# Optimization experiments

Hardware: AMD Instinct MI355X
Metric: run time of the kernel (lower is better)

The kernel has to match this reference:

```python
import jax, jax.numpy as jnp
import numpy as np

B, C, H, W = 16, 256, 64, 64
OUT_C = 3
N_TOKENS = 512
N_RES = 3
RED = 4
CB = C // RED  # bottleneck channels in ResChain
DN = ('NCHW', 'OIHW', 'NCHW')


def _conv(x, w, pad):
    return jax.lax.conv_general_dilated(x, w, (1, 1), pad, dimension_numbers=DN)


def setup_inputs() -> dict:
    key = jax.random.key(0)
    ks = jax.random.split(key, 8)
    return {
        'input': jax.random.normal(ks[0], (B, C, H, W), jnp.float32),
        'embed': jax.random.normal(ks[1], (C, N_TOKENS), jnp.float32),  # Quantize codebook [dim, n_embed]
        'res_w1': jax.random.normal(ks[2], (N_RES, CB, C, 3, 3), jnp.float32) * 0.02,
        'res_b1': jnp.zeros((N_RES, CB), jnp.float32),
        'res_w2': jax.random.normal(ks[3], (N_RES, C, CB, 1, 1), jnp.float32) * 0.02,
        'res_b2': jnp.zeros((N_RES, C), jnp.float32),
        'out_w': jax.random.normal(ks[4], (OUT_C, C, 1, 1), jnp.float32) * 0.02,
        'out_b': jnp.zeros((OUT_C,), jnp.float32),
    }


def reference(input, embed, res_w1, res_b1, res_w2, res_b2, out_w, out_b):
    sg = jax.lax.stop_gradient
    # --- Quantize (VQ-VAE codebook lookup, straight-through) ---
    x = jnp.transpose(input, (0, 2, 3, 1))  # [B,H,W,C]
    flat = x.reshape(-1, C)                  # [N, C]
    # squared L2 distance to each code: ||f||^2 - 2 f.e + ||e||^2
    dist = (flat * flat).sum(-1, keepdims=True) - 2.0 * (flat @ embed) + (embed * embed).sum(0)
    idx = jnp.argmin(dist, axis=-1).reshape(B, H, W)        # [B,H,W] int
    quantize = jnp.take(embed.T, idx, axis=0)               # embed_code: [B,H,W,C]
    diff = jnp.mean((sg(quantize) - x) ** 2)
    quantize = x + sg(quantize - x)                         # straight-through
    q = jnp.transpose(quantize, (0, 3, 1, 2))               # [B,C,H,W]
    # --- dec: ResChain(n_res_block) + 1x1 conv ---
    for i in range(N_RES):
        h = jax.nn.relu(q)
        h = _conv(h, res_w1[i], 'SAME') + res_b1[i][None, :, None, None]
        h = jax.nn.relu(h)
        h = _conv(h, res_w2[i], 'VALID') + res_b2[i][None, :, None, None]
        q = q + h
    quant = _conv(q, out_w, 'VALID') + out_b[None, :, None, None]  # [B,OUT_C,H,W]
    # --- wordfreq: per-batch bincount over idx (no grad) ---
    flat_idx = idx.reshape(B, -1)
    seg = (flat_idx + jnp.arange(B, dtype=flat_idx.dtype)[:, None] * N_TOKENS).reshape(-1)
    counts = jax.ops.segment_sum(jnp.ones_like(seg, jnp.float32), seg, num_segments=B * N_TOKENS)
    wordfreq = counts.reshape(B, N_TOKENS) / float(H * W)
    return quant, diff.reshape(1), wordfreq
```

## Files before the change

### kernel.cpp

```cpp
#include <hip/hip_runtime.h>


typedef __attribute__((ext_vector_type(8))) short short8;
typedef __attribute__((ext_vector_type(16))) float f32x16;
typedef __attribute__((ext_vector_type(8))) _Float16 half8;
typedef __attribute__((ext_vector_type(2))) _Float16 half2_t;
typedef unsigned short ushort_t;
typedef unsigned long long u64;

#define WS_QA    0
#define WS_QB    8388608
#define WS_ET    16777216
#define WS_EN    16842752
#define WS_EPK   16843264
#define WS_W1PK  16908800
#define WS_W2PK  17129984
#define WS_DIFF  17154560
#define WS_TOK   17154568
#define WS_DST   17220104
#define WS_FN    17285640
#define WS_WL    17351176

#define MARGIN 0.12f

__device__ inline ushort_t f2bf(float f) {
  unsigned u = __float_as_uint(f);
  return (ushort_t)((u + 0x7fffu + ((u >> 16) & 1u)) >> 16);
}
__device__ inline float bf2f(ushort_t h) { return __uint_as_float(((unsigned)h) << 16); }
union HU { _Float16 h; ushort_t u; };
union S8H { short8 s; half8 h; half2_t h2[4]; };

__global__ __launch_bounds__(256) void prep_kernel(
    const float* __restrict__ embed, const float* __restrict__ w1,
    const float* __restrict__ w2, float* __restrict__ ws, float* __restrict__ wf) {
  int i = blockIdx.x * 256 + threadIdx.x;
  if (i < 131072) {
    int t = i >> 8, c = i & 255;
    ((ushort_t*)(ws + WS_ET))[i] = f2bf(embed[c * 512 + t]);
  }
  if (i < 512) {
    float s = 0.f;
    for (int c = 0; c < 256; ++c) { float v = embed[c * 512 + i]; s += v * v; }
    ws[WS_EN + i] = s;
  }
  if (i < 131072) {
    int j = i & 7, lane = (i >> 3) & 63, at = (i >> 9) & 15, ks = i >> 13;
    int code = at * 32 + (lane & 31);
    int c = ks * 16 + (lane >> 5) * 8 + j;
    HU cv; cv.h = (_Float16)embed[c * 512 + code];
    ((ushort_t*)(ws + WS_EPK))[i] = cv.u;
  }
  if (i < 442368) {
    int j = i & 7; int lane = (i >> 3) & 63; int of = (i >> 9) & 1;
    int k16 = (i >> 10) & 15; int rest = i >> 14;
    int tap = rest % 9; int layer = rest / 9;
    int oc = of * 32 + (lane & 31);
    int c = k16 * 16 + (lane >> 5) * 8 + j;
    ((ushort_t*)(ws + WS_W1PK))[i] = f2bf(w1[((layer * 64 + oc) * 256 + c) * 9 + tap]);
  }
  if (i < 49152) {
    int j = i & 7, lane = (i >> 3) & 63, at = (i >> 9) & 7, ks = (i >> 12) & 3, l = i >> 14;
    int co = at * 32 + (lane & 31), cb = ks * 16 + (lane >> 5) * 8 + j;
    ((ushort_t*)(ws + WS_W2PK))[i] = f2bf(w2[(l * 256 + co) * 64 + cb]);
  }
  if (i < 8192) wf[i] = 0.f;
  if (i == 0) { ws[WS_DIFF] = 0.f; ((int*)(ws + WS_WL))[0] = 0; }
}

__global__ __launch_bounds__(512, 4) void dist_kernel(
    const float* __restrict__ input, const half8* __restrict__ epk,
    const float* __restrict__ enorm, int* __restrict__ tok,
    float* __restrict__ dst, float* __restrict__ fnv, int* __restrict__ wl) {
  __shared__ __align__(16) ushort_t sfp[2048 * 8];
  __shared__ float senorm[512];
  __shared__ float trim1[512], trim2[512];
  __shared__ int   trii[512];

  int blk = blockIdx.x, b = blk >> 6, hw0 = (blk & 63) << 6;
  int tid = threadIdx.x, lane = tid & 63, wave = tid >> 6;
  senorm[tid] = enorm[tid];

  {
    int cg = tid >> 3, sub = tid & 7;
    int ks_s = cg >> 2, hi_s = (cg >> 1) & 1, jq = cg & 1;
    const float* src0 = input + ((size_t)(b * 256 + cg * 4)) * 4096 + hw0 + sub * 8;
    float vv[4][8];
#pragma unroll
    for (int m = 0; m < 4; ++m) {
      const float4* s4 = (const float4*)(src0 + (size_t)m * 4096);
      float4 aa = s4[0], bb = s4[1];
      vv[m][0] = aa.x; vv[m][1] = aa.y; vv[m][2] = aa.z; vv[m][3] = aa.w;
      vv[m][4] = bb.x; vv[m][5] = bb.y; vv[m][6] = bb.z; vv[m][7] = bb.w;
    }
    u64* sfp64 = (u64*)sfp;
#pragma unroll
    for (int i = 0; i < 8; ++i) {
      int pl = sub * 8 + i;
      int bt = pl >> 5, lw = (pl & 31) + 32 * hi_s;
      u64 pk = 0;
#pragma unroll
      for (int m = 0; m < 4; ++m) {
        HU cv; cv.h = (_Float16)vv[m][i];
        pk |= ((u64)cv.u) << (16 * m);
      }
      sfp64[((bt * 16 + ks_s) * 64 + lw) * 2 + jq] = pk;
    }
  }
  __syncthreads();

  f32x16 acc[2][2];
#pragma unroll
  for (int bt = 0; bt < 2; ++bt)
#pragma unroll
    for (int a = 0; a < 2; ++a)
#pragma unroll
      for (int r = 0; r < 16; ++r) acc[bt][a][r] = 0.f;

  const short8* sfp8 = (const short8*)sfp;
  float fnp0 = 0.f, fnp1 = 0.f;
#pragma unroll 2
  for (int ks = 0; ks < 16; ++ks) {
    S8H u0, u1;
    u0.s = sfp8[ks * 64 + lane];
    u1.s = sfp8[(16 + ks) * 64 + lane];
#if __has_builtin(__builtin_amdgcn_fdot2)
#pragma unroll
    for (int k = 0; k < 4; ++k) {
      fnp0 = __builtin_amdgcn_fdot2(u0.h2[k], u0.h2[k], fnp0, false);
      fnp1 = __builtin_amdgcn_fdot2(u1.h2[k], u1.h2[k], fnp1, false);
    }
#else
#pragma unroll
    for (int k = 0; k < 8; ++k) {
      float v0 = (float)u0.h[k], v1 = (float)u1.h[k];
      fnp0 += v0 * v0; fnp1 += v1 * v1;
    }
#endif
#pragma unroll
    for (int a = 0; a < 2; ++a) {
      half8 ah = epk[(ks * 16 + wave * 2 + a) * 64 + lane];
      acc[0][a] = __builtin_amdgcn_mfma_f32_32x32x16_f16(ah, u0.h, acc[0][a], 0, 0, 0);
      acc[1][a] = __builtin_amdgcn_mfma_f32_32x32x16_f16(ah, u1.h, acc[1][a], 0, 0, 0);
    }
  }
  fnp0 += __shfl_xor(fnp0, 32, 64);
  fnp1 += __shfl_xor(fnp1, 32, 64);

  int hi5 = lane >> 5;
#pragma unroll
  for (int bt = 0; bt < 2; ++bt) {
    float m1 = 3.4e38f, m2 = 3.4e38f; int i1 = 0;
#pragma unroll
    for (int a = 0; a < 2; ++a)
#pragma unroll
      for (int r = 0; r < 16; ++r) {
        int code = (wave * 2 + a) * 32 + (r & 3) + 8 * (r >> 2) + 4 * hi5;
        float v = senorm[code] - 2.0f * acc[bt][a][r];
        if (v < m1) { m2 = m1; m1 = v; i1 = code; }
        else if (v < m2) m2 = v;
      }
    float o1 = __shfl_xor(m1, 32, 64);
    float o2 = __shfl_xor(m2, 32, 64);
    int   oi = __shfl_xor(i1, 32, 64);
    float n2 = fminf(fmaxf(m1, o1), fminf(m2, o2));
    float n1 = fminf(m1, o1);
    int   ni = (o1 < m1) ? oi : i1;
    if (lane < 32) {
      int p = bt * 32 + lane;
      trim1[p * 8 + wave] = n1; trim2[p * 8 + wave] = n2; trii[p * 8 + wave] = ni;
    }
  }
  __syncthreads();

  if (wave == 0) {
    int p = lane;
    float m1 = trim1[p * 8], m2 = trim2[p * 8]; int i1 = trii[p * 8];
#pragma unroll
    for (int w = 1; w < 8; ++w) {
      float a1 = trim1[p * 8 + w], a2 = trim2[p * 8 + w]; int ai = trii[p * 8 + w];
      float n2 = fminf(fmaxf(m1, a1), fminf(m2, a2));
      if (a1 < m1) { m1 = a1; i1 = ai; }
      m2 = n2;
    }
    float myfn = (lane < 32) ? fnp0 : fnp1;
    int gpos = blk * 64 + p;
    tok[gpos] = i1;
    dst[gpos] = myfn + m1;
    fnv[gpos] = myfn;
    bool flag = (m2 - m1 < MARGIN);
    u64 mk = __ballot(flag);
    int base = 0;
    if (lane == 0 && mk) base = atomicAdd(wl, (int)__popcll(mk));
    base = __shfl(base, 0, 64);
    if (flag) {
      int off = (int)__popcll(mk & ((1ull << lane) - 1ull));
      wl[1 + base + off] = gpos;
    }
  }
}

__global__ __launch_bounds__(256) void redo_kernel(
    const float* __restrict__ input, const float* __restrict__ embed,
    const float* __restrict__ enorm, const int* __restrict__ wl,
    int* __restrict__ tok, float* __restrict__ dst, const float* __restrict__ fnv) {
  __shared__ float sf[256], rv[256];
  __shared__ int   ri[256];
  int n = wl[0];
  int tid = threadIdx.x;
  for (int e = blockIdx.x; e < n; e += gridDim.x) {
    int gpos = wl[1 + e];
    int b = gpos >> 12, hw = gpos & 4095;
    sf[tid] = input[((size_t)(b * 256 + tid)) * 4096 + hw];
    __syncthreads();
    float d0 = 0.f, d1 = 0.f;
#pragma unroll 4
    for (int c = 0; c < 256; ++c) {
      float fv = sf[c];
      d0 += fv * embed[c * 512 + tid];
      d1 += fv * embed[c * 512 + 256 + tid];
    }
    float v0 = enorm[tid] - 2.f * d0;
    float v1 = enorm[256 + tid] - 2.f * d1;
    float bv; int bi;
    if (v1 < v0) { bv = v1; bi = 256 + tid; } else { bv = v0; bi = tid; }
    rv[tid] = bv; ri[tid] = bi;
    __syncthreads();
    for (int s = 128; s > 0; s >>= 1) {
      if (tid < s) {
        float ov = rv[tid + s]; int oi2 = ri[tid + s];
        if (ov < rv[tid] || (ov == rv[tid] && oi2 < ri[tid])) { rv[tid] = ov; ri[tid] = oi2; }
      }
      __syncthreads();
    }
    if (tid == 0) { tok[gpos] = ri[0]; dst[gpos] = fnv[gpos] + rv[0]; }
    __syncthreads();
  }
}

__global__ __launch_bounds__(256) void finalize_kernel(
    const int* __restrict__ tok, const float* __restrict__ dst,
    const ushort_t* __restrict__ embedT, float* __restrict__ wf,
    float* __restrict__ diffp, ushort_t* __restrict__ qout) {
  int blk = blockIdx.x;
  int tid = threadIdx.x, lane = tid & 63, wave = tid >> 6;
  int gbase = blk * 64;
  int b = gbase >> 12;
  if (wave == 0) {
    int t = tok[gbase + lane];
    atomicAdd(&wf[b * 512 + t], 1.0f / 4096.0f);
    float d = dst[gbase + lane];
#pragma unroll
    for (int off = 32; off >= 1; off >>= 1) d += __shfl_down(d, off, 64);
    if (lane == 0) atomicAdd(diffp, d);
  }
#pragma unroll 1
  for (int j = 0; j < 16; ++j) {
    int p = wave * 16 + j;
    int t = __builtin_amdgcn_readfirstlane(tok[gbase + p]);
    const u64* src = (const u64*)(embedT + (size_t)t * 256);
    u64* dstp = (u64*)(qout + ((size_t)(gbase + p)) * 256);
    dstp[lane] = src[lane];
  }
}

__global__ __launch_bounds__(512, 4) void fused_layer(
    const ushort_t* __restrict__ qin, ushort_t* __restrict__ qout,
    const ushort_t* __restrict__ w1pk, const float* __restrict__ b1,
    const ushort_t* __restrict__ w2pk, const float* __restrict__ b2, int l) {
  __shared__ __align__(16) char arena[38912];
  ushort_t* hbuf   = (ushort_t*)arena;
  float*    sb2    = (float*)(arena + 9728);
  short8*   stg    = (short8*)(arena + 10752);
  float*    red    = (float*)(arena + 10752);
  ushort_t* qstage = (ushort_t*)(arena + 10752);

  int blk = blockIdx.x;
  int b = blk >> 6; int t = blk & 63;
  int ty0 = (t >> 3) << 3;
  int tx0 = (t & 7) << 3;
  int tid = threadIdx.x, lane = tid & 63, w = tid >> 6;
  int pt = w & 1, ot = (w >> 1) & 1, kh = w >> 2;
  int l31 = lane & 31, kb5 = lane >> 5;

  if (tid < 256) sb2[tid] = b2[l * 256 + tid];

  const short8* wp  = (const short8*)w1pk + (size_t)l * 18432;
  const short8* w2p = (const short8*)w2pk;

  short8 sreg[2];
  auto loadch = [&](int cs) {
#pragma unroll
    for (int s = 0; s < 2; ++s) {
      int u = s * 512 + tid;
      if (u < 800) {
        int cg = u & 7; int pix = u >> 3; int y = pix / 10; int x = pix - y * 10;
        int sy = ty0 + y - 1, sx = tx0 + x - 1;
        if (sy >= 0 && sy < 64 && sx >= 0 && sx < 64) {
          sreg[s] = *(const short8*)(qin + ((size_t)(b * 4096 + sy * 64 + sx)) * 256 + cs * 64 + cg * 8);
        } else {
          short8 z;
#pragma unroll
          for (int k2 = 0; k2 < 8; ++k2) z[k2] = 0;
          sreg[s] = z;
        }
      }
    }
  };
  auto writech = [&](int buf) {
#pragma unroll
    for (int s = 0; s < 2; ++s) {
      int u = s * 512 + tid;
      if (u < 800) {
        int cg = u & 7; int pix = u >> 3; int y = pix / 10; int x = pix - y * 10;
        short8 sv = sreg[s];
#pragma unroll
        for (int k2 = 0; k2 < 8; ++k2) if (sv[k2] < 0) sv[k2] = 0;
        stg[buf * 880 + (y * 8 + cg) * 11 + x] = sv;
      }
    }
  };

  f32x16 acc;
#pragma unroll
  for (int r = 0; r < 16; ++r) acc[r] = 0.f;

  int py0 = pt * 4 + (l31 >> 3);
  int px0 = lane & 7;

  loadch(0);
  writech(0);
#pragma unroll 1
  for (int cs = 0; cs < 4; ++cs) {
    __syncthreads();
    if (cs < 3) loadch(cs + 1);
    int buf = cs & 1;
#pragma unroll 1
    for (int dy = 0; dy < 3; ++dy) {
#pragma unroll 1
      for (int dx = 0; dx < 3; ++dx) {
        int tap = dy * 3 + dx;
#pragma unroll
        for (int ks2 = 0; ks2 < 2; ++ks2) {
          int kk = kh * 2 + ks2;
          short8 A = stg[buf * 880 + ((py0 + dy) * 8 + kk * 2 + kb5) * 11 + px0 + dx];
          short8 B = wp[(tap * 16 + cs * 4 + kk) * 128 + ot * 64 + lane];
          acc = __builtin_amdgcn_mfma_f32_32x32x16_bf16(A, B, acc, 0, 0, 0);
        }
      }
    }
    if (cs < 3) writech((cs + 1) & 1);
  }
  __syncthreads();

  if (kh == 1) {
    float4* d = (float4*)(red + (w & 3) * 1024 + lane * 16);
#pragma unroll
    for (int r4 = 0; r4 < 4; ++r4) {
      float4 v; v.x = acc[r4 * 4]; v.y = acc[r4 * 4 + 1];
      v.z = acc[r4 * 4 + 2]; v.w = acc[r4 * 4 + 3];
      d[r4] = v;
    }
  }
  __syncthreads();
  if (kh == 0) {
    const float* s = red + (w & 3) * 1024 + lane * 16;
    int oc = ot * 32 + l31;
    float bb = b1[l * 64 + oc];
#pragma unroll
    for (int r = 0; r < 16; ++r) {
      int row = (r & 3) + 8 * (r >> 2) + 4 * kb5;
      hbuf[(pt * 32 + row) * 76 + oc] = f2bf(fmaxf(acc[r] + s[r] + bb, 0.f));
    }
  }
  __syncthreads();

  int pt2 = w & 1, coq = w >> 1;
#pragma unroll 1
  for (int ch = 0; ch < 2; ++ch) {
    short8 qv[2];
#pragma unroll
    for (int it = 0; it < 2; ++it) {
      int u = it * 512 + tid;
      int p = u >> 4, c8 = u & 15;
      int gy = ty0 + (p >> 3), gx = tx0 + (p & 7);
      qv[it] = *(const short8*)(qin + ((size_t)(b * 4096 + gy * 64 + gx)) * 256 + ch * 128 + c8 * 8);
    }

    f32x16 acc2;
#pragma unroll
    for (int r = 0; r < 16; ++r) acc2[r] = 0.f;
#pragma unroll
    for (int ks = 0; ks < 4; ++ks) {
      short8 A = *(const short8*)(hbuf + (pt2 * 32 + l31) * 76 + ks * 16 + kb5 * 8);
      short8 B = w2p[((l * 4 + ks) * 8 + ch * 4 + coq) * 64 + lane];
      acc2 = __builtin_amdgcn_mfma_f32_32x32x16_bf16(A, B, acc2, 0, 0, 0);
    }
    {
      int cc = coq * 32 + l31;
      float bb2 = sb2[ch * 128 + cc];
#pragma unroll
      for (int r = 0; r < 16; ++r) {
        int row = (r & 3) + 8 * (r >> 2) + 4 * kb5;
        qstage[(pt2 * 32 + row) * 136 + cc] = f2bf(acc2[r] + bb2);
      }
    }
    __syncthreads();
#pragma unroll
    for (int it = 0; it < 2; ++it) {
      int u = it * 512 + tid;
      int p = u >> 4, c8 = u & 15;
      short8 hv = *(const short8*)(qstage + p * 136 + c8 * 8);
      int gy = ty0 + (p >> 3), gx = tx0 + (p & 7);
      size_t gidx = ((size_t)(b * 4096 + gy * 64 + gx)) * 256 + ch * 128 + c8 * 8;
      short8 ov;
#pragma unroll
      for (int k2 = 0; k2 < 8; ++k2)
        ov[k2] = (short)f2bf(bf2f((ushort_t)qv[it][k2]) + bf2f((ushort_t)hv[k2]));
      *(short8*)(qout + gidx) = ov;
    }
    __syncthreads();
  }
}

__global__ __launch_bounds__(256) void final_kernel(
    const ushort_t* __restrict__ qbuf, const float* __restrict__ ow,
    const float* __restrict__ ob, float* __restrict__ out,
    const float* __restrict__ ws) {
  int t = blockIdx.x * 256 + threadIdx.x;
  int pos = t >> 4, c16 = t & 15;
  const ushort_t* qp = qbuf + (size_t)pos * 256 + c16 * 16;
  short8 v0 = *(const short8*)qp;
  short8 v1 = *(const short8*)(qp + 8);
  float a0 = 0.f, a1 = 0.f, a2 = 0.f;
#pragma unroll
  for (int k = 0; k < 16; ++k) {
    float f = bf2f((ushort_t)(k < 8 ? v0[k] : v1[k - 8]));
    int c = c16 * 16 + k;
    a0 += f * ow[c];
    a1 += f * ow[256 + c];
    a2 += f * ow[512 + c];
  }
#pragma unroll
  for (int off = 1; off < 16; off <<= 1) {
    a0 += __shfl_xor(a0, off, 64);
    a1 += __shfl_xor(a1, off, 64);
    a2 += __shfl_xor(a2, off, 64);
  }
  if (c16 == 0) {
    int b = pos >> 12, hw = pos & 4095;
    out[(b * 3 + 0) * 4096 + hw] = a0 + ob[0];
    out[(b * 3 + 1) * 4096 + hw] = a1 + ob[1];
    out[(b * 3 + 2) * 4096 + hw] = a2 + ob[2];
  }
  if (t == 0) out[196608] = ws[WS_DIFF] * (1.0f / 16777216.0f);
}

extern "C" void kernel_launch(void* const* d_in, const int* in_sizes, int n_in,
                              void* d_out, int out_size, void* d_ws, size_t ws_size,
                              hipStream_t stream) {
  (void)in_sizes; (void)n_in; (void)out_size; (void)ws_size;
  const float* input = (const float*)d_in[0];
  const float* embed = (const float*)d_in[1];
  const float* b1 = (const float*)d_in[3];
  const float* b2 = (const float*)d_in[5];
  const float* ow = (const float*)d_in[6];
  const float* ob = (const float*)d_in[7];
  float* ws = (float*)d_ws;
  float* out = (float*)d_out;
  float* wf = out + 196609;

  ushort_t* qA = (ushort_t*)(ws + WS_QA);
  ushort_t* qB = (ushort_t*)(ws + WS_QB);
  const ushort_t* et = (const ushort_t*)(ws + WS_ET);
  const half8* epk = (const half8*)(ws + WS_EPK);
  const ushort_t* w1pk = (const ushort_t*)(ws + WS_W1PK);
  const ushort_t* w2pk = (const ushort_t*)(ws + WS_W2PK);
  int*   tok = (int*)(ws + WS_TOK);
  float* dst = ws + WS_DST;
  float* fnv = ws + WS_FN;
  int*   wl  = (int*)(ws + WS_WL);

  hipLaunchKernelGGL(prep_kernel, dim3(1728), dim3(256), 0, stream,
                     embed, (const float*)d_in[2], (const float*)d_in[4], ws, wf);
  hipLaunchKernelGGL(dist_kernel, dim3(1024), dim3(512), 0, stream,
                     input, epk, ws + WS_EN, tok, dst, fnv, wl);
  hipLaunchKernelGGL(redo_kernel, dim3(1024), dim3(256), 0, stream,
                     input, embed, ws + WS_EN, wl, tok, dst, fnv);
  hipLaunchKernelGGL(finalize_kernel, dim3(1024), dim3(256), 0, stream,
                     tok, dst, et, wf, ws + WS_DIFF, qA);
  hipLaunchKernelGGL(fused_layer, dim3(1024), dim3(512), 0, stream,
                     qA, qB, w1pk, b1, w2pk, b2, 0);
  hipLaunchKernelGGL(fused_layer, dim3(1024), dim3(512), 0, stream,
                     qB, qA, w1pk, b1, w2pk, b2, 1);
  hipLaunchKernelGGL(fused_layer, dim3(1024), dim3(512), 0, stream,
                     qA, qB, w1pk, b1, w2pk, b2, 2);
  hipLaunchKernelGGL(final_kernel, dim3(4096), dim3(256), 0, stream,
                     qB, ow, ob, out, ws);
}
```

Before: 229.8 us.

## Replace first residual 3x3 conv with per-token lookup table of conv contributions

Since the first layer's input is a quantized codebook vector per pixel, the 3x3 conv of relu(q) is precomputed as a LUT [token][tap][oc] by a new small kernel, and layer 0 sums nine LUT rows per pixel instead of running the MFMA conv. This removes the bulk of layer-0 conv FLOPs in exchange for a serial LUT build (128 blocks over 256 channels) and gather-style LUT reads. Zero padding is handled by skipping out-of-bounds taps. fp32 accumulation of bf16-rounded embed values changes rounding slightly compared with the bf16 MFMA path.

```diff
diff --git a/kernel.cpp b/kernel.cpp
--- a/kernel.cpp
+++ b/kernel.cpp
@@ -20,6 +20,7 @@
 #define WS_DST   17220104
 #define WS_FN    17285640
 #define WS_WL    17351176
+#define WS_LUT   17416720
 
 #define MARGIN 0.12f
 
@@ -66,6 +67,26 @@
   }
   if (i < 8192) wf[i] = 0.f;
   if (i == 0) { ws[WS_DIFF] = 0.f; ((int*)(ws + WS_WL))[0] = 0; }
+}
+
+__global__ __launch_bounds__(256) void lut_kernel(
+    const float* __restrict__ embed, const float* __restrict__ w1,
+    float* __restrict__ lut) {
+  int g = blockIdx.x * 256 + threadIdx.x;
+  int t = g & 511, oc = g >> 9;
+  float acc[9];
+#pragma unroll
+  for (int tap = 0; tap < 9; ++tap) acc[tap] = 0.f;
+#pragma unroll 4
+  for (int c = 0; c < 256; ++c) {
+    float v = fmaxf(bf2f(f2bf(embed[c * 512 + t])), 0.f);
+    const float* wr = w1 + (size_t)(oc * 256 + c) * 9;
+#pragma unroll
+    for (int tap = 0; tap < 9; ++tap) acc[tap] += v * wr[tap];
+  }
+#pragma unroll
+  for (int tap = 0; tap < 9; ++tap)
+    lut[((size_t)t * 9 + tap) * 64 + oc] = acc[tap];
 }
 
 __global__ __launch_bounds__(512, 4) void dist_kernel(
@@ -264,6 +285,111 @@
   }
 }
 
+__global__ __launch_bounds__(512, 4) void layer0_kernel(
+    const ushort_t* __restrict__ qin, ushort_t* __restrict__ qout,
+    const int* __restrict__ tok, const float* __restrict__ lut,
+    const float* __restrict__ b1, const ushort_t* __restrict__ w2pk,
+    const float* __restrict__ b2) {
+  __shared__ __align__(16) char arena[28672];
+  ushort_t* hbuf   = (ushort_t*)arena;
+  float*    sb2    = (float*)(arena + 9728);
+  int*      stok   = (int*)(arena + 10752);
+  ushort_t* qstage = (ushort_t*)(arena + 11264);
+
+  int blk = blockIdx.x;
+  int b = blk >> 6; int t = blk & 63;
+  int ty0 = (t >> 3) << 3;
+  int tx0 = (t & 7) << 3;
+  int tid = threadIdx.x, lane = tid & 63, w = tid >> 6;
+  int l31 = lane & 31, kb5 = lane >> 5;
+
+  if (tid < 256) sb2[tid] = b2[tid];
+  if (tid < 100) {
+    int yy = tid / 10, xx = tid - yy * 10;
+    int sy = ty0 + yy - 1, sx = tx0 + xx - 1;
+    stok[tid] = (sy >= 0 && sy < 64 && sx >= 0 && sx < 64)
+              ? tok[b * 4096 + sy * 64 + sx] : -1;
+  }
+  __syncthreads();
+
+  {
+    int px = tid >> 3, oc8 = tid & 7;
+    int y = px >> 3, x = px & 7;
+    float a[8];
+    const float* bp = b1 + oc8 * 8;
+#pragma unroll
+    for (int j = 0; j < 8; ++j) a[j] = bp[j];
+#pragma unroll
+    for (int dy = 0; dy < 3; ++dy)
+#pragma unroll
+      for (int dx = 0; dx < 3; ++dx) {
+        int tt = stok[(y + dy) * 10 + (x + dx)];
+        if (tt >= 0) {
+          const float4* r = (const float4*)(lut + ((size_t)tt * 9 + dy * 3 + dx) * 64 + oc8 * 8);
+          float4 v0 = r[0], v1 = r[1];
+          a[0] += v0.x; a[1] += v0.y; a[2] += v0.z; a[3] += v0.w;
+          a[4] += v1.x; a[5] += v1.y; a[6] += v1.z; a[7] += v1.w;
+        }
+      }
+    u64 p0 = 0, p1 = 0;
+#pragma unroll
+    for (int j = 0; j < 4; ++j) p0 |= ((u64)f2bf(fmaxf(a[j], 0.f))) << (16 * j);
+#pragma unroll
+    for (int j = 0; j < 4; ++j) p1 |= ((u64)f2bf(fmaxf(a[4 + j], 0.f))) << (16 * j);
+    *(u64*)(hbuf + px * 76 + oc8 * 8) = p0;
+    *(u64*)(hbuf + px * 76 + oc8 * 8 + 4) = p1;
+  }
+  __syncthreads();
+
+  const short8* w2p = (const short8*)w2pk;
+  int pt2 = w & 1, coq = w >> 1;
+#pragma unroll 1
+  for (int ch = 0; ch < 2; ++ch) {
+    short8 qv[2];
+#pragma unroll
+    for (int it = 0; it < 2; ++it) {
+      int u = it * 512 + tid;
+      int p = u >> 4, c8 = u & 15;
+      int gy = ty0 + (p >> 3), gx = tx0 + (p & 7);
+      qv[it] = *(const short8*)(qin + ((size_t)(b * 4096 + gy * 64 + gx)) * 256 + ch * 128 + c8 * 8);
+    }
+
+    f32x16 acc2;
+#pragma unroll
+    for (int r = 0; r < 16; ++r) acc2[r] = 0.f;
+#pragma unroll
+    for (int ks = 0; ks < 4; ++ks) {
+      short8 A = *(const short8*)(hbuf + (pt2 * 32 + l31) * 76 + ks * 16 + kb5 * 8);
+      short8 B = w2p[(ks * 8 + ch * 4 + coq) * 64 + lane];
+      acc2 = __builtin_amdgcn_mfma_f32_32x32x16_bf16(A, B, acc2, 0, 0, 0);
+    }
+    {
+      int cc = coq * 32 + l31;
+      float bb2 = sb2[ch * 128 + cc];
+#pragma unroll
+      for (int r = 0; r < 16; ++r) {
+        int row = (r & 3) + 8 * (r >> 2) + 4 * kb5;
+        qstage[(pt2 * 32 + row) * 136 + cc] = f2bf(acc2[r] + bb2);
+      }
+    }
+    __syncthreads();
+#pragma unroll
+    for (int it = 0; it < 2; ++it) {
+      int u = it * 512 + tid;
+      int p = u >> 4, c8 = u & 15;
+      short8 hv = *(const short8*)(qstage + p * 136 + c8 * 8);
+      int gy = ty0 + (p >> 3), gx = tx0 + (p & 7);
+      size_t gidx = ((size_t)(b * 4096 + gy * 64 + gx)) * 256 + ch * 128 + c8 * 8;
+      short8 ov;
+#pragma unroll
+      for (int k2 = 0; k2 < 8; ++k2)
+        ov[k2] = (short)f2bf(bf2f((ushort_t)qv[it][k2]) + bf2f((ushort_t)hv[k2]));
+      *(short8*)(qout + gidx) = ov;
+    }
+    __syncthreads();
+  }
+}
+
 __global__ __launch_bounds__(512, 4) void fused_layer(
     const ushort_t* __restrict__ qin, ushort_t* __restrict__ qout,
     const ushort_t* __restrict__ w1pk, const float* __restrict__ b1,
@@ -462,6 +588,7 @@
   (void)in_sizes; (void)n_in; (void)out_size; (void)ws_size;
   const float* input = (const float*)d_in[0];
   const float* embed = (const float*)d_in[1];
+  const float* w1 = (const float*)d_in[2];
   const float* b1 = (const float*)d_in[3];
   const float* b2 = (const float*)d_in[5];
   const float* ow = (const float*)d_in[6];
@@ -480,17 +607,20 @@
   float* dst = ws + WS_DST;
   float* fnv = ws + WS_FN;
   int*   wl  = (int*)(ws + WS_WL);
+  float* lut = ws + WS_LUT;
 
   hipLaunchKernelGGL(prep_kernel, dim3(1728), dim3(256), 0, stream,
-                     embed, (const float*)d_in[2], (const float*)d_in[4], ws, wf);
+                     embed, w1, (const float*)d_in[4], ws, wf);
+  hipLaunchKernelGGL(lut_kernel, dim3(128), dim3(256), 0, stream,
+                     embed, w1, lut);
   hipLaunchKernelGGL(dist_kernel, dim3(1024), dim3(512), 0, stream,
                      input, epk, ws + WS_EN, tok, dst, fnv, wl);
   hipLaunchKernelGGL(redo_kernel, dim3(1024), dim3(256), 0, stream,
                      input, embed, ws + WS_EN, wl, tok, dst, fnv);
   hipLaunchKernelGGL(finalize_kernel, dim3(1024), dim3(256), 0, stream,
                      tok, dst, et, wf, ws + WS_DIFF, qA);
-  hipLaunchKernelGGL(fused_layer, dim3(1024), dim3(512), 0, stream,
-                     qA, qB, w1pk, b1, w2pk, b2, 0);
+  hipLaunchKernelGGL(layer0_kernel, dim3(1024), dim3(512), 0, stream,
+                     qA, qB, tok, lut, b1, w2pk, b2);
   hipLaunchKernelGGL(fused_layer, dim3(1024), dim3(512), 0, stream,
                      qB, qA, w1pk, b1, w2pk, b2, 1);
   hipLaunchKernelGGL(fused_layer, dim3(1024), dim3(512), 0, stream,
```

Result: slower. 238.1 us (+3.6%).

## Stage conv input tiles via direct global-to-LDS loads with XOR swizzle

Applied to the files above, without the earlier changes.

Replaces the register-staged load-then-write of the 10x10 halo tile with __builtin_amdgcn_global_load_lds direct copies into a swizzled 16-wide LDS layout. Out-of-bounds pixels read from a zeroed page in workspace, and the ReLU moves from staging time to each A-fragment read. The aim is to drop register staging and VGPR pressure and overlap the next chunk's load with MFMA work. In exchange the LDS arena grows from about 38 KB to about 51 KB, which may lower occupancy at 4 blocks per CU, and the ReLU is now redone on every fragment read.

```diff
diff --git a/kernel.cpp b/kernel.cpp
--- a/kernel.cpp
+++ b/kernel.cpp
@@ -20,6 +20,7 @@
 #define WS_DST   17220104
 #define WS_FN    17285640
 #define WS_WL    17351176
+#define WS_ZERO  17416720
 
 #define MARGIN 0.12f
 
@@ -65,6 +66,7 @@
     ((ushort_t*)(ws + WS_W2PK))[i] = f2bf(w2[(l * 256 + co) * 64 + cb]);
   }
   if (i < 8192) wf[i] = 0.f;
+  if (i < 16) ws[WS_ZERO + i] = 0.f;
   if (i == 0) { ws[WS_DIFF] = 0.f; ((int*)(ws + WS_WL))[0] = 0; }
 }
 
@@ -267,13 +269,14 @@
 __global__ __launch_bounds__(512, 4) void fused_layer(
     const ushort_t* __restrict__ qin, ushort_t* __restrict__ qout,
     const ushort_t* __restrict__ w1pk, const float* __restrict__ b1,
-    const ushort_t* __restrict__ w2pk, const float* __restrict__ b2, int l) {
-  __shared__ __align__(16) char arena[38912];
-  ushort_t* hbuf   = (ushort_t*)arena;
-  float*    sb2    = (float*)(arena + 9728);
-  short8*   stg    = (short8*)(arena + 10752);
-  float*    red    = (float*)(arena + 10752);
-  ushort_t* qstage = (ushort_t*)(arena + 10752);
+    const ushort_t* __restrict__ w2pk, const float* __restrict__ b2,
+    const ushort_t* __restrict__ zeropage, int l) {
+  __shared__ __align__(16) char arena[51712];
+  short8*   stg8   = (short8*)arena;
+  float*    red    = (float*)arena;
+  ushort_t* qstage = (ushort_t*)arena;
+  ushort_t* hbuf   = (ushort_t*)(arena + 40960);
+  float*    sb2    = (float*)(arena + 50688);
 
   int blk = blockIdx.x;
   int b = blk >> 6; int t = blk & 63;
@@ -288,35 +291,21 @@
   const short8* wp  = (const short8*)w1pk + (size_t)l * 18432;
   const short8* w2p = (const short8*)w2pk;
 
-  short8 sreg[2];
-  auto loadch = [&](int cs) {
-#pragma unroll
-    for (int s = 0; s < 2; ++s) {
+  auto stage = [&](int cs, int buf) {
+#pragma unroll
+    for (int s = 0; s < 3; ++s) {
       int u = s * 512 + tid;
-      if (u < 800) {
-        int cg = u & 7; int pix = u >> 3; int y = pix / 10; int x = pix - y * 10;
+      if (u < 1280) {
+        int n = u ^ ((u >> 3) & 7);
+        int y = n >> 7, x = (n >> 3) & 15, cg = n & 7;
         int sy = ty0 + y - 1, sx = tx0 + x - 1;
-        if (sy >= 0 && sy < 64 && sx >= 0 && sx < 64) {
-          sreg[s] = *(const short8*)(qin + ((size_t)(b * 4096 + sy * 64 + sx)) * 256 + cs * 64 + cg * 8);
-        } else {
-          short8 z;
-#pragma unroll
-          for (int k2 = 0; k2 < 8; ++k2) z[k2] = 0;
-          sreg[s] = z;
-        }
-      }
-    }
-  };
-  auto writech = [&](int buf) {
-#pragma unroll
-    for (int s = 0; s < 2; ++s) {
-      int u = s * 512 + tid;
-      if (u < 800) {
-        int cg = u & 7; int pix = u >> 3; int y = pix / 10; int x = pix - y * 10;
-        short8 sv = sreg[s];
-#pragma unroll
-        for (int k2 = 0; k2 < 8; ++k2) if (sv[k2] < 0) sv[k2] = 0;
-        stg[buf * 880 + (y * 8 + cg) * 11 + x] = sv;
+        const ushort_t* src = zeropage;
+        if (x < 10 && sy >= 0 && sy < 64 && sx >= 0 && sx < 64)
+          src = qin + ((size_t)(b * 4096 + sy * 64 + sx)) * 256 + cs * 64 + cg * 8;
+        __builtin_amdgcn_global_load_lds(
+            (const __attribute__((address_space(1))) void*)src,
+            (__attribute__((address_space(3))) void*)(stg8 + buf * 1280 + u),
+            16, 0, 0);
       }
     }
   };
@@ -328,12 +317,11 @@
   int py0 = pt * 4 + (l31 >> 3);
   int px0 = lane & 7;
 
-  loadch(0);
-  writech(0);
+  stage(0, 0);
+  __syncthreads();
 #pragma unroll 1
   for (int cs = 0; cs < 4; ++cs) {
-    __syncthreads();
-    if (cs < 3) loadch(cs + 1);
+    if (cs < 3) stage(cs + 1, (cs + 1) & 1);
     int buf = cs & 1;
 #pragma unroll 1
     for (int dy = 0; dy < 3; ++dy) {
@@ -343,15 +331,18 @@
 #pragma unroll
         for (int ks2 = 0; ks2 < 2; ++ks2) {
           int kk = kh * 2 + ks2;
-          short8 A = stg[buf * 880 + ((py0 + dy) * 8 + kk * 2 + kb5) * 11 + px0 + dx];
+          int n_r = ((py0 + dy) * 16 + (px0 + dx)) * 8 + (kk * 2 + kb5);
+          int u_r = n_r ^ ((n_r >> 3) & 7);
+          short8 A = stg8[buf * 1280 + u_r];
+#pragma unroll
+          for (int k2 = 0; k2 < 8; ++k2) if (A[k2] < 0) A[k2] = 0;
           short8 B = wp[(tap * 16 + cs * 4 + kk) * 128 + ot * 64 + lane];
           acc = __builtin_amdgcn_mfma_f32_32x32x16_bf16(A, B, acc, 0, 0, 0);
         }
       }
     }
-    if (cs < 3) writech((cs + 1) & 1);
-  }
-  __syncthreads();
+    __syncthreads();
+  }
 
   if (kh == 1) {
     float4* d = (float4*)(red + (w & 3) * 1024 + lane * 16);
@@ -462,6 +453,7 @@
   (void)in_sizes; (void)n_in; (void)out_size; (void)ws_size;
   const float* input = (const float*)d_in[0];
   const float* embed = (const float*)d_in[1];
+  const float* w1 = (const float*)d_in[2];
   const float* b1 = (const float*)d_in[3];
   const float* b2 = (const float*)d_in[5];
   const float* ow = (const float*)d_in[6];
@@ -476,13 +468,14 @@
   const half8* epk = (const half8*)(ws + WS_EPK);
   const ushort_t* w1pk = (const ushort_t*)(ws + WS_W1PK);
   const ushort_t* w2pk = (const ushort_t*)(ws + WS_W2PK);
+  const ushort_t* zp = (const ushort_t*)(ws + WS_ZERO);
   int*   tok = (int*)(ws + WS_TOK);
   float* dst = ws + WS_DST;
   float* fnv = ws + WS_FN;
   int*   wl  = (int*)(ws + WS_WL);
 
   hipLaunchKernelGGL(prep_kernel, dim3(1728), dim3(256), 0, stream,
-                     embed, (const float*)d_in[2], (const float*)d_in[4], ws, wf);
+                     embed, w1, (const float*)d_in[4], ws, wf);
   hipLaunchKernelGGL(dist_kernel, dim3(1024), dim3(512), 0, stream,
                      input, epk, ws + WS_EN, tok, dst, fnv, wl);
   hipLaunchKernelGGL(redo_kernel, dim3(1024), dim3(256), 0, stream,
@@ -490,11 +483,11 @@
   hipLaunchKernelGGL(finalize_kernel, dim3(1024), dim3(256), 0, stream,
                      tok, dst, et, wf, ws + WS_DIFF, qA);
   hipLaunchKernelGGL(fused_layer, dim3(1024), dim3(512), 0, stream,
-                     qA, qB, w1pk, b1, w2pk, b2, 0);
+                     qA, qB, w1pk, b1, w2pk, b2, zp, 0);
   hipLaunchKernelGGL(fused_layer, dim3(1024), dim3(512), 0, stream,
-                     qB, qA, w1pk, b1, w2pk, b2, 1);
+                     qB, qA, w1pk, b1, w2pk, b2, zp, 1);
   hipLaunchKernelGGL(fused_layer, dim3(1024), dim3(512), 0, stream,
-                     qA, qB, w1pk, b1, w2pk, b2, 2);
+                     qA, qB, w1pk, b1, w2pk, b2, zp, 2);
   hipLaunchKernelGGL(final_kernel, dim3(4096), dim3(256), 0, stream,
                      qB, ow, ob, out, ws);
 }
```

Result: slower. 274.6 us (+19.5%).
